# Optimization experiments

Hardware: AMD Instinct MI355X
Metric: run time of the kernel (lower is better)

Reference implementation:

```python
import jax, jax.numpy as jnp
import numpy as np

N = 100_000        # num nodes
E = 1_600_000      # num edges (avg degree 16)
F_IN = 128         # input node feature dim
F_E = 32           # edge feature dim
D = 32             # out_dim per head
H = 4              # heads


def setup_inputs() -> dict:
    key = jax.random.key(0)
    ks = jax.random.split(key, 8)
    s = 0.05
    return {
        "node_features": jax.random.normal(ks[0], (N, F_IN), jnp.float32),
        "edge_index": jax.random.randint(ks[1], (E, 2), 0, N, jnp.int32),
        "edge_features": jax.random.normal(ks[2], (E, F_E), jnp.float32),
        "W_node": jax.random.normal(ks[3], (F_IN, D * H), jnp.float32) * s,
        "W_edge": jax.random.normal(ks[4], (F_E, D * H), jnp.float32) * s,
        "attn_kernel": jax.random.normal(ks[5], (H, 3 * D), jnp.float32) * s,
        "W_out": jax.random.normal(ks[6], (D * H, D), jnp.float32) * s,
        "b_out": jnp.zeros((D,), jnp.float32),
    }


def segment_softmax(logits, seg, num_segments):
    # logits: [E, H], seg: [E] destination node ids
    mx = jax.ops.segment_max(logits, seg, num_segments=num_segments)   # [N, H]
    ex = jnp.exp(logits - mx[seg])
    denom = jax.ops.segment_sum(ex, seg, num_segments=num_segments)    # [N, H]
    return ex / (denom[seg] + 1e-8)


def reference(node_features, edge_index, edge_features, W_node, W_edge,
              attn_kernel, W_out, b_out):
    src_idx = edge_index[:, 0]
    dst_idx = edge_index[:, 1]

    # Node / edge projections -> [*, H, D]
    node_proj = (node_features @ W_node).reshape(N, H, D)
    edge_proj = (edge_features @ W_edge).reshape(E, H, D)

    # attn_kernel is [H, 3D] applied to concat(src, dst, edge); split it so we
    # never materialize the [E, H, 3D] concat. Src/dst terms are computed
    # per-node then gathered (same math, far less traffic).
    a_src, a_dst, a_edge = attn_kernel[:, :D], attn_kernel[:, D:2 * D], attn_kernel[:, 2 * D:]
    s_src = jnp.einsum('nhd,hd->nh', node_proj, a_src)   # [N, H]
    s_dst = jnp.einsum('nhd,hd->nh', node_proj, a_dst)   # [N, H]
    s_edge = jnp.einsum('ehd,hd->eh', edge_proj, a_edge)  # [E, H]

    logits = s_src[src_idx] + s_dst[dst_idx] + s_edge     # [E, H]
    attn = segment_softmax(logits, dst_idx, N)             # [E, H]

    src_feat = node_proj[src_idx]                          # [E, H, D]
    messages = (attn[:, :, None] * src_feat).reshape(E, H * D)
    agg = jax.ops.segment_sum(messages, dst_idx, num_segments=N)  # [N, H*D]

    out = jax.nn.gelu(agg @ W_out + b_out, approximate=False)     # exact erf GELU
    return out
```

## Files before the change

kernel.cpp:

```cpp
#include <hip/hip_runtime.h>
#include <hip/hip_bf16.h>
#include <hip/hip_fp16.h>

#define F_IN 128
#define F_E  32
#define DH   128
#define HD   32

__device__ __forceinline__ unsigned short f2bf(float f) {
    unsigned int x = __float_as_uint(f);
    unsigned int r = (x + 0x7fffu + ((x >> 16) & 1u)) >> 16;
    return (unsigned short)r;
}

__global__ void prep_kernel(const float* __restrict__ W_edge,
                            const float* __restrict__ attn,
                            float* __restrict__ wefold) {
    int t = threadIdx.x;
    int f = t >> 2, h = t & 3;
    float s = 0.f;
#pragma unroll
    for (int d = 0; d < 32; ++d)
        s += W_edge[f * DH + h * HD + d] * attn[h * 96 + 64 + d];
    wefold[f * 4 + h] = s;
}

__global__ __launch_bounds__(256, 4)
void node_proj_kernel(const float* __restrict__ x, const float* __restrict__ Wn,
                      const float* __restrict__ attn,
                      unsigned short* __restrict__ proj_bf,
                      float* __restrict__ s_src, int N) {
    __shared__ float xsT[32 * 132];
    __shared__ float ws[32 * 132];
    const int t  = threadIdx.x;
    const int n0 = blockIdx.x * 128;
    const int tc = t & 15, tn = t >> 4;
    const float4* x4  = (const float4*)x;
    const float4* Wn4 = (const float4*)Wn;

    float acc[2][2][4][4];
#pragma unroll
    for (int a = 0; a < 2; ++a)
#pragma unroll
        for (int b = 0; b < 2; ++b)
#pragma unroll
            for (int i = 0; i < 4; ++i)
#pragma unroll
                for (int j = 0; j < 4; ++j) acc[a][b][i][j] = 0.f;

    for (int ch = 0; ch < 4; ++ch) {
        __syncthreads();
#pragma unroll
        for (int j = 0; j < 4; ++j) {
            int idx = t + j * 256;
            int n  = idx >> 3;
            int kq = idx & 7;
            float4 v = make_float4(0.f, 0.f, 0.f, 0.f);
            if (n0 + n < N) v = x4[(size_t)(n0 + n) * 32 + ch * 8 + kq];
            int kk = kq * 4;
            xsT[(kk + 0) * 132 + n] = v.x;
            xsT[(kk + 1) * 132 + n] = v.y;
            xsT[(kk + 2) * 132 + n] = v.z;
            xsT[(kk + 3) * 132 + n] = v.w;
        }
#pragma unroll
        for (int j = 0; j < 4; ++j) {
            int idx = t + j * 256;
            int kk = idx >> 5, cq = idx & 31;
            float4 v = Wn4[(size_t)(ch * 32 + kk) * 32 + cq];
            *(float4*)&ws[kk * 132 + cq * 4] = v;
        }
        __syncthreads();
#pragma unroll 4
        for (int kk = 0; kk < 32; ++kk) {
            float4 a0 = *(const float4*)&xsT[kk * 132 + tn * 4];
            float4 a1 = *(const float4*)&xsT[kk * 132 + 64 + tn * 4];
            float4 b0 = *(const float4*)&ws[kk * 132 + tc * 4];
            float4 b1 = *(const float4*)&ws[kk * 132 + 64 + tc * 4];
            float av[2][4] = {{a0.x, a0.y, a0.z, a0.w}, {a1.x, a1.y, a1.z, a1.w}};
            float bv[2][4] = {{b0.x, b0.y, b0.z, b0.w}, {b1.x, b1.y, b1.z, b1.w}};
#pragma unroll
            for (int ni = 0; ni < 2; ++ni)
#pragma unroll
                for (int ci = 0; ci < 2; ++ci)
#pragma unroll
                    for (int ii = 0; ii < 4; ++ii)
#pragma unroll
                        for (int jj = 0; jj < 4; ++jj)
                            acc[ni][ci][ii][jj] =
                                fmaf(av[ni][ii], bv[ci][jj], acc[ni][ci][ii][jj]);
        }
    }

    float asv[2][4];
#pragma unroll
    for (int ci = 0; ci < 2; ++ci)
#pragma unroll
        for (int jj = 0; jj < 4; ++jj) {
            int c = ci * 64 + tc * 4 + jj;
            int h = c >> 5, d = c & 31;
            asv[ci][jj] = attn[h * 96 + d];
        }

#pragma unroll
    for (int ni = 0; ni < 2; ++ni)
#pragma unroll
        for (int ii = 0; ii < 4; ++ii) {
            int n = n0 + ni * 64 + tn * 4 + ii;
            bool ok = (n < N);
            if (ok) {
                union { unsigned short h[4]; uint2 u; } p0, p1;
#pragma unroll
                for (int jj = 0; jj < 4; ++jj) {
                    p0.h[jj] = f2bf(acc[ni][0][ii][jj]);
                    p1.h[jj] = f2bf(acc[ni][1][ii][jj]);
                }
                *(uint2*)&proj_bf[(size_t)n * DH + tc * 4]      = p0.u;
                *(uint2*)&proj_bf[(size_t)n * DH + 64 + tc * 4] = p1.u;
            }
#pragma unroll
            for (int ci = 0; ci < 2; ++ci) {
                float ps = 0.f;
#pragma unroll
                for (int jj = 0; jj < 4; ++jj)
                    ps = fmaf(acc[ni][ci][ii][jj], asv[ci][jj], ps);
                ps += __shfl_xor(ps, 1);
                ps += __shfl_xor(ps, 2);
                ps += __shfl_xor(ps, 4);
                if (ok && (tc & 7) == 0) {
                    int h = ci * 2 + (tc >> 3);
                    s_src[n * 4 + h] = ps;
                }
            }
        }
}

__global__ __launch_bounds__(256)
void hist_kernel(const int* __restrict__ eidx, int* __restrict__ cnt, int E) {
    int e = blockIdx.x * 256 + threadIdx.x;
    if (e < E) {
        int d = ((const int2*)eidx)[e].y;
        atomicAdd(&cnt[d], 1);
    }
}

__global__ __launch_bounds__(256)
void scan1_kernel(const int* __restrict__ cnt, int* __restrict__ cursor,
                  int* __restrict__ bsum, int N) {
    __shared__ int s[256];
    const int t = threadIdx.x;
    int i = blockIdx.x * 256 + t;
    int v = (i < N) ? cnt[i] : 0;
    s[t] = v;
    __syncthreads();
#pragma unroll
    for (int d = 1; d < 256; d <<= 1) {
        int x = (t >= d) ? s[t - d] : 0;
        __syncthreads();
        s[t] += x;
        __syncthreads();
    }
    if (i < N) cursor[i] = s[t] - v;
    if (t == 255) bsum[blockIdx.x] = s[255];
}

__global__ __launch_bounds__(512)
void scan2_kernel(int* __restrict__ bsum, int nb) {
    __shared__ int s[512];
    const int t = threadIdx.x;
    int v = (t < nb) ? bsum[t] : 0;
    s[t] = v;
    __syncthreads();
#pragma unroll
    for (int d = 1; d < 512; d <<= 1) {
        int x = (t >= d) ? s[t - d] : 0;
        __syncthreads();
        s[t] += x;
        __syncthreads();
    }
    if (t < nb) bsum[t] = s[t] - v;
}

__global__ __launch_bounds__(256)
void scan3_kernel(int* __restrict__ cursor, const int* __restrict__ bsum, int N) {
    int i = blockIdx.x * 256 + threadIdx.x;
    if (i < N) cursor[i] += bsum[blockIdx.x];
}

__global__ __launch_bounds__(256)
void scatter_kernel(const float* __restrict__ ef, const int* __restrict__ eidx,
                    const float* __restrict__ wefold,
                    const float* __restrict__ s_src,
                    int* __restrict__ cursor, uint4* __restrict__ rec, int E) {
    __shared__ float wf[128];
    const int t = threadIdx.x;
    if (t < 128) wf[t] = wefold[t];
    __syncthreads();

    const int e = blockIdx.x * 256 + t;
    if (e >= E) return;
    int2 sd = ((const int2*)eidx)[e];
    int s_i = sd.x, d_i = sd.y;
    float es0 = 0.f, es1 = 0.f, es2 = 0.f, es3 = 0.f;
#pragma unroll
    for (int f4 = 0; f4 < 8; ++f4) {
        float4 v = *(const float4*)&ef[(size_t)e * F_E + f4 * 4];
        float vv[4] = {v.x, v.y, v.z, v.w};
#pragma unroll
        for (int q = 0; q < 4; ++q) {
            float4 wv = *(const float4*)&wf[(f4 * 4 + q) * 4];
            es0 = fmaf(vv[q], wv.x, es0);
            es1 = fmaf(vv[q], wv.y, es1);
            es2 = fmaf(vv[q], wv.z, es2);
            es3 = fmaf(vv[q], wv.w, es3);
        }
    }
    float4 a = *(const float4*)&s_src[s_i * 4];
    float w0 = __expf(a.x + es0), w1 = __expf(a.y + es1);
    float w2 = __expf(a.z + es2), w3 = __expf(a.w + es3);
    unsigned int u0 = __half_as_ushort(__float2half_rn(w0));
    unsigned int u1 = __half_as_ushort(__float2half_rn(w1));
    unsigned int u2 = __half_as_ushort(__float2half_rn(w2));
    unsigned int u3 = __half_as_ushort(__float2half_rn(w3));
    uint4 r;
    r.x = (unsigned int)s_i;
    r.y = u0 | (u1 << 16);
    r.z = u2 | (u3 << 16);
    r.w = 0u;
    int pos = atomicAdd(&cursor[d_i], 1);
    rec[pos] = r;
}

__global__ __launch_bounds__(256)
void gather_kernel(const int* __restrict__ cursor, const uint4* __restrict__ rec,
                   const unsigned int* __restrict__ proj_bf,
                   unsigned int* __restrict__ numer_bf, int N) {
    const int t    = threadIdx.x;
    const int lane = t & 63;
    const int n    = blockIdx.x * 4 + (t >> 6);
    if (n >= N) return;

    const int start = (n == 0) ? 0 : cursor[n - 1];
    const int end   = cursor[n];
    const int h     = lane >> 4;

    float2 acc = make_float2(0.f, 0.f);
    float dsum = 0.f;

    int i = start;
    for (; i + 4 <= end; i += 4) {
        uint4 r[4];
#pragma unroll
        for (int q = 0; q < 4; ++q) r[q] = rec[i + q];
        unsigned int pv[4];
#pragma unroll
        for (int q = 0; q < 4; ++q)
            pv[q] = proj_bf[(size_t)r[q].x * 64 + lane];
#pragma unroll
        for (int q = 0; q < 4; ++q) {
            unsigned int packed = (h < 2) ? r[q].y : r[q].z;
            unsigned short uw = (h & 1) ? (unsigned short)(packed >> 16)
                                        : (unsigned short)(packed & 0xffffu);
            float w = __half2float(__ushort_as_half(uw));
            dsum += w;
            acc.x = fmaf(w, __uint_as_float(pv[q] << 16), acc.x);
            acc.y = fmaf(w, __uint_as_float(pv[q] & 0xffff0000u), acc.y);
        }
    }
    for (; i < end; ++i) {
        uint4 r = rec[i];
        unsigned int u = proj_bf[(size_t)r.x * 64 + lane];
        unsigned int packed = (h < 2) ? r.y : r.z;
        unsigned short uw = (h & 1) ? (unsigned short)(packed >> 16)
                                    : (unsigned short)(packed & 0xffffu);
        float w = __half2float(__ushort_as_half(uw));
        dsum += w;
        acc.x = fmaf(w, __uint_as_float(u << 16), acc.x);
        acc.y = fmaf(w, __uint_as_float(u & 0xffff0000u), acc.y);
    }

    float r = 1.f / (dsum + 1e-8f);
    unsigned int p = (unsigned int)f2bf(acc.x * r) |
                     ((unsigned int)f2bf(acc.y * r) << 16);
    numer_bf[(size_t)n * 64 + lane] = p;
}

__global__ __launch_bounds__(256, 2)
void out_kernel(const unsigned int* __restrict__ numer_bf,
                const float* __restrict__ Wout, const float* __restrict__ bout,
                float* __restrict__ out, int N) {
    __shared__ float wsh[128 * 32];
    __shared__ float bsh[32];
    const int t = threadIdx.x;
    for (int i = t; i < 4096; i += 256) wsh[i] = Wout[i];
    if (t < 32) bsh[t] = bout[t];
    __syncthreads();

    int n = blockIdx.x * 256 + t;
    if (n >= N) return;

    float acc[32];
#pragma unroll
    for (int j = 0; j < 32; ++j) acc[j] = 0.f;

    for (int kg = 0; kg < 16; ++kg) {
        uint4 v = *(const uint4*)&numer_bf[(size_t)n * 64 + kg * 4];
        unsigned int vv[4] = {v.x, v.y, v.z, v.w};
#pragma unroll
        for (int q = 0; q < 4; ++q) {
            int k = kg * 8 + q * 2;
            float a0 = __uint_as_float(vv[q] << 16);
            float a1 = __uint_as_float(vv[q] & 0xffff0000u);
#pragma unroll
            for (int j = 0; j < 32; j += 4) {
                float4 w0 = *(const float4*)&wsh[k * 32 + j];
                float4 w1 = *(const float4*)&wsh[(k + 1) * 32 + j];
                acc[j + 0] = fmaf(a0, w0.x, fmaf(a1, w1.x, acc[j + 0]));
                acc[j + 1] = fmaf(a0, w0.y, fmaf(a1, w1.y, acc[j + 1]));
                acc[j + 2] = fmaf(a0, w0.z, fmaf(a1, w1.z, acc[j + 2]));
                acc[j + 3] = fmaf(a0, w0.w, fmaf(a1, w1.w, acc[j + 3]));
            }
        }
    }
#pragma unroll
    for (int j = 0; j < 32; ++j) {
        float z = acc[j] + bsh[j];
        acc[j] = 0.5f * z * (1.f + erff(z * 0.70710678118654752f));
    }
#pragma unroll
    for (int j = 0; j < 32; j += 4)
        *(float4*)&out[(size_t)n * 32 + j] = make_float4(acc[j], acc[j+1], acc[j+2], acc[j+3]);
}

extern "C" void kernel_launch(void* const* d_in, const int* in_sizes, int n_in,
                              void* d_out, int out_size, void* d_ws, size_t ws_size,
                              hipStream_t stream) {
    const float* x    = (const float*)d_in[0];
    const int*   eidx = (const int*)d_in[1];
    const float* ef   = (const float*)d_in[2];
    const float* Wn   = (const float*)d_in[3];
    const float* We   = (const float*)d_in[4];
    const float* attn = (const float*)d_in[5];
    const float* Wout = (const float*)d_in[6];
    const float* bout = (const float*)d_in[7];
    float* out = (float*)d_out;

    const int N = in_sizes[0] / F_IN;
    const int E = in_sizes[1] / 2;
    const int NB = (N + 255) / 256;

    char* ws = (char*)d_ws;
    size_t off = 0;
    auto alloc = [&](size_t bytes) {
        void* p = ws + off;
        off = (off + bytes + 255) & ~(size_t)255;
        return p;
    };
    int*   cnt     = (int*)  alloc((size_t)N * 4);
    size_t zero_bytes = off;
    int*   cursor  = (int*)  alloc((size_t)N * 4);
    int*   bsum    = (int*)  alloc(512 * 4);
    float* wefold  = (float*)alloc(512);
    float* s_src   = (float*)alloc((size_t)N * 4 * 4);
    unsigned short* proj_bf = (unsigned short*)alloc((size_t)N * DH * 2);
    unsigned int*   numer_bf = (unsigned int*)alloc((size_t)N * 64 * 4);
    uint4* rec     = (uint4*)alloc((size_t)E * 16);

    hipMemsetAsync(d_ws, 0, zero_bytes, stream);
    hipLaunchKernelGGL(prep_kernel, dim3(1), dim3(128), 0, stream, We, attn, wefold);
    hipLaunchKernelGGL(hist_kernel, dim3((E + 255) / 256), dim3(256), 0, stream,
                       eidx, cnt, E);
    hipLaunchKernelGGL(scan1_kernel, dim3(NB), dim3(256), 0, stream, cnt, cursor, bsum, N);
    hipLaunchKernelGGL(scan2_kernel, dim3(1), dim3(512), 0, stream, bsum, NB);
    hipLaunchKernelGGL(scan3_kernel, dim3(NB), dim3(256), 0, stream, cursor, bsum, N);
    hipLaunchKernelGGL(node_proj_kernel, dim3((N + 127) / 128), dim3(256), 0, stream,
                       x, Wn, attn, proj_bf, s_src, N);
    hipLaunchKernelGGL(scatter_kernel, dim3((E + 255) / 256), dim3(256), 0, stream,
                       ef, eidx, wefold, s_src, cursor, rec, E);
    hipLaunchKernelGGL(gather_kernel, dim3((N + 3) / 4), dim3(256), 0, stream,
                       cursor, rec, (const unsigned int*)proj_bf, numer_bf, N);
    hipLaunchKernelGGL(out_kernel, dim3((N + 255) / 256), dim3(256), 0, stream,
                       numer_bf, Wout, bout, out, N);
}
```

Before: 609.5 us.

## Fuse histogram into edge prep and place records via atomic-returned ranks

Edge logit computation moves into a pass that also performs the degree histogram, using each atomicAdd's return value as the edge's rank within its destination. Records are staged per edge, then a later scatter places them at cursor+rank without atomics. This removes the second atomic pass and the separate histogram pass, at the cost of an extra write and read of a per-edge staging buffer. The buffer is aliased with the numerator buffer. Packing assumes node ids fit in 17 bits and degrees below 32768.

```diff
diff --git a/kernel.cpp b/kernel.cpp
--- a/kernel.cpp
+++ b/kernel.cpp
@@ -136,12 +136,47 @@
 }
 
 __global__ __launch_bounds__(256)
-void hist_kernel(const int* __restrict__ eidx, int* __restrict__ cnt, int E) {
-    int e = blockIdx.x * 256 + threadIdx.x;
-    if (e < E) {
-        int d = ((const int2*)eidx)[e].y;
-        atomicAdd(&cnt[d], 1);
-    }
+void edgeprep_kernel(const float* __restrict__ ef, const int* __restrict__ eidx,
+                     const float* __restrict__ wefold,
+                     const float* __restrict__ s_src,
+                     int* __restrict__ cnt, uint4* __restrict__ rec_e, int E) {
+    __shared__ float wf[128];
+    const int t = threadIdx.x;
+    if (t < 128) wf[t] = wefold[t];
+    __syncthreads();
+
+    const int e = blockIdx.x * 256 + t;
+    if (e >= E) return;
+    int2 sd = ((const int2*)eidx)[e];
+    int s_i = sd.x, d_i = sd.y;
+    float es0 = 0.f, es1 = 0.f, es2 = 0.f, es3 = 0.f;
+#pragma unroll
+    for (int f4 = 0; f4 < 8; ++f4) {
+        float4 v = *(const float4*)&ef[(size_t)e * F_E + f4 * 4];
+        float vv[4] = {v.x, v.y, v.z, v.w};
+#pragma unroll
+        for (int q = 0; q < 4; ++q) {
+            float4 wv = *(const float4*)&wf[(f4 * 4 + q) * 4];
+            es0 = fmaf(vv[q], wv.x, es0);
+            es1 = fmaf(vv[q], wv.y, es1);
+            es2 = fmaf(vv[q], wv.z, es2);
+            es3 = fmaf(vv[q], wv.w, es3);
+        }
+    }
+    float4 a = *(const float4*)&s_src[s_i * 4];
+    float w0 = __expf(a.x + es0), w1 = __expf(a.y + es1);
+    float w2 = __expf(a.z + es2), w3 = __expf(a.w + es3);
+    unsigned int u0 = __half_as_ushort(__float2half_rn(w0));
+    unsigned int u1 = __half_as_ushort(__float2half_rn(w1));
+    unsigned int u2 = __half_as_ushort(__float2half_rn(w2));
+    unsigned int u3 = __half_as_ushort(__float2half_rn(w3));
+    int r = atomicAdd(&cnt[d_i], 1);
+    uint4 R;
+    R.x = (unsigned int)s_i;
+    R.y = u0 | (u1 << 16);
+    R.z = u2 | (u3 << 16);
+    R.w = ((unsigned int)d_i << 15) | (unsigned int)r;
+    rec_e[e] = R;
 }
 
 __global__ __launch_bounds__(256)
@@ -188,60 +223,29 @@
 }
 
 __global__ __launch_bounds__(256)
-void scatter_kernel(const float* __restrict__ ef, const int* __restrict__ eidx,
-                    const float* __restrict__ wefold,
-                    const float* __restrict__ s_src,
-                    int* __restrict__ cursor, uint4* __restrict__ rec, int E) {
-    __shared__ float wf[128];
-    const int t = threadIdx.x;
-    if (t < 128) wf[t] = wefold[t];
-    __syncthreads();
-
-    const int e = blockIdx.x * 256 + t;
+void scatter_kernel(const uint4* __restrict__ rec_e,
+                    const int* __restrict__ cursor,
+                    uint4* __restrict__ rec, int E) {
+    const int e = blockIdx.x * 256 + threadIdx.x;
     if (e >= E) return;
-    int2 sd = ((const int2*)eidx)[e];
-    int s_i = sd.x, d_i = sd.y;
-    float es0 = 0.f, es1 = 0.f, es2 = 0.f, es3 = 0.f;
-#pragma unroll
-    for (int f4 = 0; f4 < 8; ++f4) {
-        float4 v = *(const float4*)&ef[(size_t)e * F_E + f4 * 4];
-        float vv[4] = {v.x, v.y, v.z, v.w};
-#pragma unroll
-        for (int q = 0; q < 4; ++q) {
-            float4 wv = *(const float4*)&wf[(f4 * 4 + q) * 4];
-            es0 = fmaf(vv[q], wv.x, es0);
-            es1 = fmaf(vv[q], wv.y, es1);
-            es2 = fmaf(vv[q], wv.z, es2);
-            es3 = fmaf(vv[q], wv.w, es3);
-        }
-    }
-    float4 a = *(const float4*)&s_src[s_i * 4];
-    float w0 = __expf(a.x + es0), w1 = __expf(a.y + es1);
-    float w2 = __expf(a.z + es2), w3 = __expf(a.w + es3);
-    unsigned int u0 = __half_as_ushort(__float2half_rn(w0));
-    unsigned int u1 = __half_as_ushort(__float2half_rn(w1));
-    unsigned int u2 = __half_as_ushort(__float2half_rn(w2));
-    unsigned int u3 = __half_as_ushort(__float2half_rn(w3));
-    uint4 r;
-    r.x = (unsigned int)s_i;
-    r.y = u0 | (u1 << 16);
-    r.z = u2 | (u3 << 16);
-    r.w = 0u;
-    int pos = atomicAdd(&cursor[d_i], 1);
-    rec[pos] = r;
+    uint4 R = rec_e[e];
+    int d = (int)(R.w >> 15);
+    int r = (int)(R.w & 32767u);
+    int pos = cursor[d] + r;
+    rec[pos] = R;
 }
 
 __global__ __launch_bounds__(256)
 void gather_kernel(const int* __restrict__ cursor, const uint4* __restrict__ rec,
                    const unsigned int* __restrict__ proj_bf,
-                   unsigned int* __restrict__ numer_bf, int N) {
+                   unsigned int* __restrict__ numer_bf, int N, int E) {
     const int t    = threadIdx.x;
     const int lane = t & 63;
     const int n    = blockIdx.x * 4 + (t >> 6);
     if (n >= N) return;
 
-    const int start = (n == 0) ? 0 : cursor[n - 1];
-    const int end   = cursor[n];
+    const int start = cursor[n];
+    const int end   = (n == N - 1) ? E : cursor[n + 1];
     const int h     = lane >> 4;
 
     float2 acc = make_float2(0.f, 0.f);
@@ -363,22 +367,26 @@
     float* wefold  = (float*)alloc(512);
     float* s_src   = (float*)alloc((size_t)N * 4 * 4);
     unsigned short* proj_bf = (unsigned short*)alloc((size_t)N * DH * 2);
-    unsigned int*   numer_bf = (unsigned int*)alloc((size_t)N * 64 * 4);
+    size_t numer_bytes = (size_t)N * 64 * 4;
+    size_t rece_bytes  = (size_t)E * 16;
+    unsigned int* numer_bf = (unsigned int*)alloc(numer_bytes > rece_bytes ?
+                                                  numer_bytes : rece_bytes);
+    uint4* rec_e   = (uint4*)numer_bf;
     uint4* rec     = (uint4*)alloc((size_t)E * 16);
 
     hipMemsetAsync(d_ws, 0, zero_bytes, stream);
     hipLaunchKernelGGL(prep_kernel, dim3(1), dim3(128), 0, stream, We, attn, wefold);
-    hipLaunchKernelGGL(hist_kernel, dim3((E + 255) / 256), dim3(256), 0, stream,
-                       eidx, cnt, E);
+    hipLaunchKernelGGL(node_proj_kernel, dim3((N + 127) / 128), dim3(256), 0, stream,
+                       x, Wn, attn, proj_bf, s_src, N);
+    hipLaunchKernelGGL(edgeprep_kernel, dim3((E + 255) / 256), dim3(256), 0, stream,
+                       ef, eidx, wefold, s_src, cnt, rec_e, E);
     hipLaunchKernelGGL(scan1_kernel, dim3(NB), dim3(256), 0, stream, cnt, cursor, bsum, N);
     hipLaunchKernelGGL(scan2_kernel, dim3(1), dim3(512), 0, stream, bsum, NB);
     hipLaunchKernelGGL(scan3_kernel, dim3(NB), dim3(256), 0, stream, cursor, bsum, N);
-    hipLaunchKernelGGL(node_proj_kernel, dim3((N + 127) / 128), dim3(256), 0, stream,
-                       x, Wn, attn, proj_bf, s_src, N);
     hipLaunchKernelGGL(scatter_kernel, dim3((E + 255) / 256), dim3(256), 0, stream,
-                       ef, eidx, wefold, s_src, cursor, rec, E);
+                       rec_e, cursor, rec, E);
     hipLaunchKernelGGL(gather_kernel, dim3((N + 3) / 4), dim3(256), 0, stream,
-                       cursor, rec, (const unsigned int*)proj_bf, numer_bf, N);
+                       cursor, rec, (const unsigned int*)proj_bf, numer_bf, N, E);
     hipLaunchKernelGGL(out_kernel, dim3((N + 255) / 256), dim3(256), 0, stream,
                        numer_bf, Wout, bout, out, N);
 }
```

New measurement: 546.4 us. 1.12x faster.
